# Kernel tuning notes

Measured on AMD Instinct MI355X. Metric: run time of the kernel, lower is better.

## Reference

```python
import jax, jax.numpy as jnp
import numpy as np

N_NODES = 100000
ORDER = 2


def _spmm(edge_src, edge_dst, edge_weight, x):
    # out[dst] += w * x[src]  ==  adj @ x  with adj in COO form
    msgs = edge_weight[:, None] * x[edge_src]          # [E, d]
    return jax.ops.segment_sum(msgs, edge_dst, num_segments=N_NODES)


def setup_inputs() -> dict:
    key = jax.random.key(0)
    k1, k2, k3, k4 = jax.random.split(key, 4)
    x = jax.random.normal(k1, (N_NODES, 32), dtype=jnp.float32)
    edge_src = jax.random.randint(k2, (1600000,), 0, N_NODES, dtype=jnp.int32)
    edge_dst = jax.random.randint(k3, (1600000,), 0, N_NODES, dtype=jnp.int32)
    edge_weight = jax.random.uniform(k4, (1600000,), dtype=jnp.float32)
    return {"x": x, "edge_src": edge_src, "edge_dst": edge_dst,
            "edge_weight": edge_weight}


def reference(x, edge_src, edge_dst, edge_weight):
    # SGConvolution.forward: x = spmm(adj, x) repeated `order` times
    for _ in range(ORDER):
        x = _spmm(edge_src, edge_dst, edge_weight, x)
    return x
```

## Files before the change

kernel.cpp:

```cpp
#include <hip/hip_runtime.h>

#define N_NODES 100000
#define NEDGE   1600000
#define D       32

#define BSHIFT   8
#define BNODES   256
#define NBUCKET  ((N_NODES + BNODES - 1) / BNODES)
#define NB_PAD   392
#define EPB      4096
#define EPT      (EPB / 256)
#define CBLK     ((NEDGE + EPB - 1) / EPB)
#define CAP      5120

__global__ void init_cur_kernel(int* __restrict__ bucket_cur) {
    int i = blockIdx.x * blockDim.x + threadIdx.x;
    if (i < NB_PAD) bucket_cur[i] = i * CAP;
}

__global__ __launch_bounds__(256) void bin_edges_kernel(
        const int* __restrict__ src, const int* __restrict__ dst,
        const float* __restrict__ w,
        int* __restrict__ bucket_cur, int2* __restrict__ binned) {
    __shared__ int2 sorted[EPB];
    __shared__ unsigned short bucketOf[EPB];
    __shared__ int cnt[NB_PAD];
    __shared__ int ndoff[NB_PAD];
    __shared__ int delta[NB_PAD];
    __shared__ int partial[256];

    const int tid = threadIdx.x;
    const int e0  = blockIdx.x * EPB;
    const int total = min(EPB, NEDGE - e0);

    for (int i = tid; i < NB_PAD; i += 256) cnt[i] = 0;
    __syncthreads();

    int myd[EPT];
    #pragma unroll
    for (int it = 0; it < EPT; ++it) {
        int e = e0 + it * 256 + tid;
        myd[it] = (e < NEDGE) ? dst[e] : -1;
        if (myd[it] >= 0) atomicAdd(&cnt[myd[it] >> BSHIFT], 1);
    }
    __syncthreads();

    {
        int b0 = tid * 2;
        int c0 = 0, c1 = 0, s = 0;
        if (b0 < NB_PAD) { c0 = cnt[b0]; c1 = cnt[b0 + 1]; s = c0 + c1; }
        partial[tid] = s;
        __syncthreads();
        int v = s;
        for (int o = 1; o < 256; o <<= 1) {
            int t2 = (tid >= o) ? partial[tid - o] : 0;
            __syncthreads();
            partial[tid] += t2;
            __syncthreads();
        }
        int run = partial[tid] - v;
        if (b0 < NB_PAD) {
            ndoff[b0] = run;
            if (c0 > 0) delta[b0] = atomicAdd(&bucket_cur[b0], c0) - run;
            cnt[b0] = 0;
            run += c0;
            ndoff[b0 + 1] = run;
            if (c1 > 0) delta[b0 + 1] = atomicAdd(&bucket_cur[b0 + 1], c1) - run;
            cnt[b0 + 1] = 0;
            run += c1;
        }
    }
    __syncthreads();

    #pragma unroll
    for (int it = 0; it < EPT; ++it) {
        int d = myd[it];
        if (d >= 0) {
            int e = e0 + it * 256 + tid;
            int b = d >> BSHIFT;
            int r = atomicAdd(&cnt[b], 1);
            int loc = ndoff[b] + r;
            sorted[loc]   = make_int2(src[e] | ((d & (BNODES - 1)) << 17),
                                      __float_as_int(w[e]));
            bucketOf[loc] = (unsigned short)b;
        }
    }
    __syncthreads();

    for (int i = tid; i < total; i += 256) {
        int2 v = sorted[i];
        int  b = bucketOf[i];
        binned[delta[b] + i] = v;
    }
}

__global__ __launch_bounds__(256) void build_csr_kernel(
        const int* __restrict__ bucket_cur,
        int2* __restrict__ binned, int* __restrict__ offv, int* __restrict__ deg) {
    __shared__ int2 sorted[CAP];
    __shared__ int ndcnt[BNODES];
    __shared__ int ndoff[BNODES];

    int b = blockIdx.x;
    int tid = threadIdx.x;
    int start = b * CAP;
    int cnt_b = min(bucket_cur[b] - start, CAP);

    ndcnt[tid] = 0;
    __syncthreads();

    for (int i = tid; i < cnt_b; i += 256)
        atomicAdd(&ndcnt[(binned[start + i].x >> 17) & (BNODES - 1)], 1);
    __syncthreads();

    int v = ndcnt[tid];
    ndoff[tid] = v;
    __syncthreads();
    for (int o = 1; o < BNODES; o <<= 1) {
        int t = (tid >= o) ? ndoff[tid - o] : 0;
        __syncthreads();
        ndoff[tid] += t;
        __syncthreads();
    }
    {
        int incl = ndoff[tid];
        __syncthreads();
        ndoff[tid] = incl - v;
        int node = b * BNODES + tid;
        if (node < N_NODES) {
            offv[node] = start + incl - v;
            deg[node]  = v;
        }
        ndcnt[tid] = 0;
    }
    __syncthreads();

    for (int i = tid; i < cnt_b; i += 256) {
        int2 p = binned[start + i];
        int dl = (p.x >> 17) & (BNODES - 1);
        int r = atomicAdd(&ndcnt[dl], 1);
        sorted[ndoff[dl] + r] = make_int2(p.x & 0x1FFFF, p.y);
    }
    __syncthreads();
    for (int i = tid; i < cnt_b; i += 256) binned[start + i] = sorted[i];
}

__global__ void spmm_gather_kernel(const int* __restrict__ off, const int* __restrict__ deg,
                                   const int2* __restrict__ csr_sw,
                                   const float* __restrict__ x, float* __restrict__ out) {
    int gid = blockIdx.x * blockDim.x + threadIdx.x;
    if (gid >= N_NODES * 8) return;
    int node = gid >> 3;
    int c    = gid & 7;
    int start = off[node];
    int len   = deg[node];
    float4 acc = {0.f, 0.f, 0.f, 0.f};
    int k = 0;
    for (; k + 4 <= len; k += 4) {
        int2 sw0 = csr_sw[start + k];
        int2 sw1 = csr_sw[start + k + 1];
        int2 sw2 = csr_sw[start + k + 2];
        int2 sw3 = csr_sw[start + k + 3];
        const float4 xv0 = *reinterpret_cast<const float4*>(&x[(long)sw0.x * D + c * 4]);
        const float4 xv1 = *reinterpret_cast<const float4*>(&x[(long)sw1.x * D + c * 4]);
        const float4 xv2 = *reinterpret_cast<const float4*>(&x[(long)sw2.x * D + c * 4]);
        const float4 xv3 = *reinterpret_cast<const float4*>(&x[(long)sw3.x * D + c * 4]);
        float w0 = __int_as_float(sw0.y), w1 = __int_as_float(sw1.y);
        float w2 = __int_as_float(sw2.y), w3 = __int_as_float(sw3.y);
        acc.x += w0 * xv0.x; acc.y += w0 * xv0.y; acc.z += w0 * xv0.z; acc.w += w0 * xv0.w;
        acc.x += w1 * xv1.x; acc.y += w1 * xv1.y; acc.z += w1 * xv1.z; acc.w += w1 * xv1.w;
        acc.x += w2 * xv2.x; acc.y += w2 * xv2.y; acc.z += w2 * xv2.z; acc.w += w2 * xv2.w;
        acc.x += w3 * xv3.x; acc.y += w3 * xv3.y; acc.z += w3 * xv3.z; acc.w += w3 * xv3.w;
    }
    for (; k < len; ++k) {
        int2 sw = csr_sw[start + k];
        const float4 xv = *reinterpret_cast<const float4*>(&x[(long)sw.x * D + c * 4]);
        float wt = __int_as_float(sw.y);
        acc.x += wt * xv.x; acc.y += wt * xv.y; acc.z += wt * xv.z; acc.w += wt * xv.w;
    }
    *reinterpret_cast<float4*>(&out[(long)node * D + c * 4]) = acc;
}

__global__ void spmm_scatter_kernel(const int* __restrict__ src, const int* __restrict__ dst,
                                    const float* __restrict__ w, const float* __restrict__ x,
                                    float* __restrict__ out) {
    long gid = (long)blockIdx.x * blockDim.x + threadIdx.x;
    if (gid >= (long)NEDGE * 8) return;
    int e = (int)(gid >> 3);
    int c = (int)(gid & 7);
    int s = src[e], d = dst[e];
    float wt = w[e];
    const float4 xv = *reinterpret_cast<const float4*>(&x[(long)s * D + c * 4]);
    float* o = &out[(long)d * D + c * 4];
    atomicAdd(o + 0, wt * xv.x);
    atomicAdd(o + 1, wt * xv.y);
    atomicAdd(o + 2, wt * xv.z);
    atomicAdd(o + 3, wt * xv.w);
}

extern "C" void kernel_launch(void* const* d_in, const int* in_sizes, int n_in,
                              void* d_out, int out_size, void* d_ws, size_t ws_size,
                              hipStream_t stream) {
    const float* x    = (const float*)d_in[0];
    const int*   esrc = (const int*)d_in[1];
    const int*   edst = (const int*)d_in[2];
    const float* ew   = (const float*)d_in[3];
    float* out = (float*)d_out;

    char* ws = (char*)d_ws;
    const size_t y_bytes   = (size_t)N_NODES * D * sizeof(float);
    const size_t n_ints    = (size_t)N_NODES * sizeof(int);
    const size_t b_ints    = (size_t)NB_PAD * sizeof(int);
    const size_t arena_sz  = (size_t)NBUCKET * CAP * sizeof(int2);

    size_t o = 0;
    float* y          = (float*)(ws + o); o += y_bytes;
    int2*  binned     = (int2*) (ws + o); o += arena_sz;
    int*   off        = (int*)  (ws + o); o += n_ints;
    int*   deg        = (int*)  (ws + o); o += n_ints;
    int*   bucket_cur = (int*)  (ws + o); o += b_ints;

    if (ws_size < o) {
        hipMemsetAsync(y, 0, y_bytes, stream);
        hipMemsetAsync(out, 0, y_bytes, stream);
        const long total = (long)NEDGE * 8;
        const int blocks = (int)((total + 255) / 256);
        spmm_scatter_kernel<<<blocks, 256, 0, stream>>>(esrc, edst, ew, x, y);
        spmm_scatter_kernel<<<blocks, 256, 0, stream>>>(esrc, edst, ew, y, out);
        return;
    }

    init_cur_kernel<<<2, 256, 0, stream>>>(bucket_cur);
    bin_edges_kernel<<<CBLK, 256, 0, stream>>>(esrc, edst, ew, bucket_cur, binned);
    build_csr_kernel<<<NBUCKET, 256, 0, stream>>>(bucket_cur, binned, off, deg);

    const int gblocks = (N_NODES * 8 + 255) / 256;
    spmm_gather_kernel<<<gblocks, 256, 0, stream>>>(off, deg, binned, x, y);
    spmm_gather_kernel<<<gblocks, 256, 0, stream>>>(off, deg, binned, y, out);
}
```

Before: 112.1 us.

## Sort nodes by degree within buckets and unroll gather loop by eight

The CSR build kernel now counting-sorts the nodes of each 256-node bucket by degree (capped at 63) and writes a node permutation. The gather kernel walks that permutation, so threads in a wavefront handle nodes of similar degree, which reduces divergence from uneven row lengths. The inner loop also gains an 8-way unrolled stage that issues more independent gathers per iteration. Costs are an extra scan in the build kernel, an indirect node lookup, scattered output writes, and higher register pressure.

```diff
diff --git a/kernel.cpp b/kernel.cpp
--- a/kernel.cpp
+++ b/kernel.cpp
@@ -8,6 +8,7 @@
 #define BNODES   256
 #define NBUCKET  ((N_NODES + BNODES - 1) / BNODES)
 #define NB_PAD   392
+#define NPOS     (NBUCKET * BNODES)
 #define EPB      4096
 #define EPT      (EPB / 256)
 #define CBLK     ((NEDGE + EPB - 1) / EPB)
@@ -96,10 +97,13 @@
 
 __global__ __launch_bounds__(256) void build_csr_kernel(
         const int* __restrict__ bucket_cur,
-        int2* __restrict__ binned, int* __restrict__ offv, int* __restrict__ deg) {
+        int2* __restrict__ binned, int* __restrict__ offv, int* __restrict__ deg,
+        int* __restrict__ norder) {
     __shared__ int2 sorted[CAP];
     __shared__ int ndcnt[BNODES];
     __shared__ int ndoff[BNODES];
+    __shared__ int dcnt[64];
+    __shared__ int dscan[64];
 
     int b = blockIdx.x;
     int tid = threadIdx.x;
@@ -122,16 +126,38 @@
         ndoff[tid] += t;
         __syncthreads();
     }
+    int node = b * BNODES + tid;
     {
         int incl = ndoff[tid];
         __syncthreads();
         ndoff[tid] = incl - v;
-        int node = b * BNODES + tid;
         if (node < N_NODES) {
             offv[node] = start + incl - v;
             deg[node]  = v;
         }
         ndcnt[tid] = 0;
+    }
+    __syncthreads();
+
+    {
+        if (tid < 64) dcnt[tid] = 0;
+        __syncthreads();
+        int dkey = (node < N_NODES) ? min(v, 63) : 0;
+        atomicAdd(&dcnt[dkey], 1);
+        __syncthreads();
+        int dv = (tid < 64) ? dcnt[tid] : 0;
+        if (tid < 64) dscan[tid] = dv;
+        __syncthreads();
+        for (int o = 1; o < 64; o <<= 1) {
+            int t = (tid < 64 && tid >= o) ? dscan[tid - o] : 0;
+            __syncthreads();
+            if (tid < 64) dscan[tid] += t;
+            __syncthreads();
+        }
+        if (tid < 64) { dscan[tid] -= dv; dcnt[tid] = 0; }
+        __syncthreads();
+        int pos = dscan[dkey] + atomicAdd(&dcnt[dkey], 1);
+        norder[b * BNODES + pos] = node;
     }
     __syncthreads();
 
@@ -145,32 +171,44 @@
     for (int i = tid; i < cnt_b; i += 256) binned[start + i] = sorted[i];
 }
 
-__global__ void spmm_gather_kernel(const int* __restrict__ off, const int* __restrict__ deg,
-                                   const int2* __restrict__ csr_sw,
-                                   const float* __restrict__ x, float* __restrict__ out) {
+__global__ __launch_bounds__(256) void spmm_gather_kernel(
+        const int* __restrict__ off, const int* __restrict__ deg,
+        const int* __restrict__ norder, const int2* __restrict__ csr_sw,
+        const float* __restrict__ x, float* __restrict__ out) {
     int gid = blockIdx.x * blockDim.x + threadIdx.x;
-    if (gid >= N_NODES * 8) return;
-    int node = gid >> 3;
+    if (gid >= NPOS * 8) return;
+    int node = norder[gid >> 3];
+    if (node >= N_NODES) return;
     int c    = gid & 7;
     int start = off[node];
     int len   = deg[node];
     float4 acc = {0.f, 0.f, 0.f, 0.f};
     int k = 0;
+    for (; k + 8 <= len; k += 8) {
+        int2 sw[8];
+        #pragma unroll
+        for (int j = 0; j < 8; ++j) sw[j] = csr_sw[start + k + j];
+        float4 xv[8];
+        #pragma unroll
+        for (int j = 0; j < 8; ++j)
+            xv[j] = *reinterpret_cast<const float4*>(&x[(long)sw[j].x * D + c * 4]);
+        #pragma unroll
+        for (int j = 0; j < 8; ++j) {
+            float wt = __int_as_float(sw[j].y);
+            acc.x += wt * xv[j].x; acc.y += wt * xv[j].y;
+            acc.z += wt * xv[j].z; acc.w += wt * xv[j].w;
+        }
+    }
     for (; k + 4 <= len; k += 4) {
-        int2 sw0 = csr_sw[start + k];
-        int2 sw1 = csr_sw[start + k + 1];
-        int2 sw2 = csr_sw[start + k + 2];
-        int2 sw3 = csr_sw[start + k + 3];
-        const float4 xv0 = *reinterpret_cast<const float4*>(&x[(long)sw0.x * D + c * 4]);
-        const float4 xv1 = *reinterpret_cast<const float4*>(&x[(long)sw1.x * D + c * 4]);
-        const float4 xv2 = *reinterpret_cast<const float4*>(&x[(long)sw2.x * D + c * 4]);
-        const float4 xv3 = *reinterpret_cast<const float4*>(&x[(long)sw3.x * D + c * 4]);
-        float w0 = __int_as_float(sw0.y), w1 = __int_as_float(sw1.y);
-        float w2 = __int_as_float(sw2.y), w3 = __int_as_float(sw3.y);
-        acc.x += w0 * xv0.x; acc.y += w0 * xv0.y; acc.z += w0 * xv0.z; acc.w += w0 * xv0.w;
-        acc.x += w1 * xv1.x; acc.y += w1 * xv1.y; acc.z += w1 * xv1.z; acc.w += w1 * xv1.w;
-        acc.x += w2 * xv2.x; acc.y += w2 * xv2.y; acc.z += w2 * xv2.z; acc.w += w2 * xv2.w;
-        acc.x += w3 * xv3.x; acc.y += w3 * xv3.y; acc.z += w3 * xv3.z; acc.w += w3 * xv3.w;
+        int2 sw[4];
+        #pragma unroll
+        for (int j = 0; j < 4; ++j) sw[j] = csr_sw[start + k + j];
+        #pragma unroll
+        for (int j = 0; j < 4; ++j) {
+            const float4 xv = *reinterpret_cast<const float4*>(&x[(long)sw[j].x * D + c * 4]);
+            float wt = __int_as_float(sw[j].y);
+            acc.x += wt * xv.x; acc.y += wt * xv.y; acc.z += wt * xv.z; acc.w += wt * xv.w;
+        }
     }
     for (; k < len; ++k) {
         int2 sw = csr_sw[start + k];
@@ -210,6 +248,7 @@
     char* ws = (char*)d_ws;
     const size_t y_bytes   = (size_t)N_NODES * D * sizeof(float);
     const size_t n_ints    = (size_t)N_NODES * sizeof(int);
+    const size_t p_ints    = (size_t)NPOS * sizeof(int);
     const size_t b_ints    = (size_t)NB_PAD * sizeof(int);
     const size_t arena_sz  = (size_t)NBUCKET * CAP * sizeof(int2);
 
@@ -218,6 +257,7 @@
     int2*  binned     = (int2*) (ws + o); o += arena_sz;
     int*   off        = (int*)  (ws + o); o += n_ints;
     int*   deg        = (int*)  (ws + o); o += n_ints;
+    int*   norder     = (int*)  (ws + o); o += p_ints;
     int*   bucket_cur = (int*)  (ws + o); o += b_ints;
 
     if (ws_size < o) {
@@ -232,9 +272,9 @@
 
     init_cur_kernel<<<2, 256, 0, stream>>>(bucket_cur);
     bin_edges_kernel<<<CBLK, 256, 0, stream>>>(esrc, edst, ew, bucket_cur, binned);
-    build_csr_kernel<<<NBUCKET, 256, 0, stream>>>(bucket_cur, binned, off, deg);
-
-    const int gblocks = (N_NODES * 8 + 255) / 256;
-    spmm_gather_kernel<<<gblocks, 256, 0, stream>>>(off, deg, binned, x, y);
-    spmm_gather_kernel<<<gblocks, 256, 0, stream>>>(off, deg, binned, y, out);
-}
+    build_csr_kernel<<<NBUCKET, 256, 0, stream>>>(bucket_cur, binned, off, deg, norder);
+
+    const int gblocks = (NPOS * 8 + 255) / 256;
+    spmm_gather_kernel<<<gblocks, 256, 0, stream>>>(off, deg, norder, binned, x, y);
+    spmm_gather_kernel<<<gblocks, 256, 0, stream>>>(off, deg, norder, binned, y, out);
+}
```

Measured after the change: 128.0 us. 1.14x slower.
